# Kernel tuning notes

Hardware: AMD Instinct MI355X
Metric: run time of the kernel (lower is better)

The kernel has to match this reference:

```python
import jax, jax.numpy as jnp
import numpy as np

EPS = 1e-5
NUM_HEADS = 16
HEAD_DIM = 64


def layernorm(x, g, b):
    mu = jnp.mean(x, axis=-1, keepdims=True)
    var = jnp.mean(jnp.square(x - mu), axis=-1, keepdims=True)
    return (x - mu) * jax.lax.rsqrt(var + EPS) * g + b


def setup_inputs() -> dict:
    key = jax.random.key(0)
    ks = jax.random.split(key, 10)
    B, S, Q, D = 4, 4096, 256, 1024
    x = jax.random.normal(ks[0], (B, S, D), dtype=jnp.float32)
    queries = jax.random.normal(ks[1], (B, Q, D), dtype=jnp.float32)
    attn_mask = jax.random.randint(ks[2], (B, NUM_HEADS, Q, S), 0, 2) == 1
    key_padding_mask = jax.random.randint(ks[3], (B, S), 0, 2) == 1
    scale = 1.0 / np.sqrt(2.0 * D)  # xavier-ish
    Wq = jax.random.normal(ks[4], (D, D), dtype=jnp.float32) * scale
    Wk = jax.random.normal(ks[5], (D, D), dtype=jnp.float32) * scale
    Wv = jax.random.normal(ks[6], (D, D), dtype=jnp.float32) * scale
    Wo = jax.random.normal(ks[7], (D, D), dtype=jnp.float32) * scale
    ln1_g = jnp.ones((D,), jnp.float32); ln1_b = jnp.zeros((D,), jnp.float32)
    ln2_g = jnp.ones((D,), jnp.float32); ln2_b = jnp.zeros((D,), jnp.float32)
    return {"x": x, "queries": queries, "attn_mask": attn_mask,
            "key_padding_mask": key_padding_mask, "Wq": Wq, "Wk": Wk,
            "Wv": Wv, "Wo": Wo, "ln1_g": ln1_g, "ln1_b": ln1_b,
            "ln2_g": ln2_g, "ln2_b": ln2_b}


def reference(x, queries, attn_mask, key_padding_mask, Wq, Wk, Wv, Wo,
              ln1_g, ln1_b, ln2_g, ln2_b):
    B, S, D = x.shape
    Q = queries.shape[1]
    H, hd = NUM_HEADS, HEAD_DIM

    xn = layernorm(x, ln1_g, ln1_b)
    q = (queries @ Wq.T).reshape(B, Q, H, hd)
    k = (xn @ Wk.T).reshape(B, S, H, hd)
    v = (xn @ Wv.T).reshape(B, S, H, hd)

    # scores: (B, H, Q, S)
    scores = jnp.einsum('bqhd,bshd->bhqs', q, k) / np.sqrt(hd)

    mask = attn_mask | key_padding_mask[:, None, None, :]
    neg_inf = jnp.float32(-jnp.inf)
    masked = jnp.where(mask, neg_inf, scores)
    all_masked = jnp.all(mask, axis=-1, keepdims=True)  # rows fully masked
    safe = jnp.where(all_masked, 0.0, masked)
    attn = jax.nn.softmax(safe, axis=-1)
    attn = jnp.where(all_masked, 0.0, attn)

    out = jnp.einsum('bhqs,bshd->bqhd', attn, v).reshape(B, Q, D)
    out = layernorm(out, ln2_g, ln2_b)
    return out @ Wo.T, attn.mean(axis=1)
```

## Files before the change

kernel.cpp:

```cpp
#include <hip/hip_runtime.h>
#include <math.h>

#define DEV __device__ __forceinline__

typedef float  f4v  __attribute__((ext_vector_type(4)));
typedef __bf16 b8v  __attribute__((ext_vector_type(8)));
typedef short  s8v  __attribute__((ext_vector_type(8)));

DEV short f2b(float f){ __bf16 h = (__bf16)f; return __builtin_bit_cast(short, h); }
DEV float b2f(short s){ __bf16 h = __builtin_bit_cast(__bf16, s); return (float)h; }

DEV void gload16(const void* g, void* l){
  __builtin_amdgcn_global_load_lds((const __attribute__((address_space(1))) void*)g,
                                   (__attribute__((address_space(3))) void*)l, 16, 0, 0);
}

DEV b8v ldsf(const short* p){ return __builtin_bit_cast(b8v, *(const s8v*)p); }

DEV f4v mfma16(b8v a, b8v b, f4v c){ return __builtin_amdgcn_mfma_f32_16x16x32_bf16(a, b, c, 0, 0, 0); }

DEV void lds_barrier(){
  asm volatile("s_waitcnt lgkmcnt(0)" ::: "memory");
  __builtin_amdgcn_s_barrier();
}

__global__ void cvt5_kernel(const float* __restrict__ s0, const float* __restrict__ s1,
                            const float* __restrict__ s2, const float* __restrict__ s3,
                            const float* __restrict__ s4,
                            short* __restrict__ d0, short* __restrict__ d1,
                            short* __restrict__ d2, short* __restrict__ d3,
                            short* __restrict__ d4){
  int i = blockIdx.x*256 + threadIdx.x;
  int buf = i >> 18, j = i & 262143;
  const float* s = (buf==0)?s0:(buf==1)?s1:(buf==2)?s2:(buf==3)?s3:s4;
  short*       d = (buf==0)?d0:(buf==1)?d1:(buf==2)?d2:(buf==3)?d3:d4;
  float4 v = ((const float4*)s)[j];
  ((short4*)d)[j] = make_short4(f2b(v.x), f2b(v.y), f2b(v.z), f2b(v.w));
}

__global__ __launch_bounds__(256) void ln_kernel(const float* __restrict__ x, const float* __restrict__ gg,
                                                 const float* __restrict__ bb, short* __restrict__ out){
  int row = blockIdx.x, tid = threadIdx.x;
  const float4 v = ((const float4*)(x + (size_t)row*1024))[tid];
  float s = v.x + v.y + v.z + v.w;
  #pragma unroll
  for (int off=1; off<64; off<<=1) s += __shfl_xor(s, off);
  __shared__ float red[4];
  if ((tid&63)==0) red[tid>>6] = s;
  __syncthreads();
  float mu = (red[0]+red[1]+red[2]+red[3]) * (1.0f/1024.0f);
  float d0=v.x-mu, d1=v.y-mu, d2=v.z-mu, d3=v.w-mu;
  float q = d0*d0 + d1*d1 + d2*d2 + d3*d3;
  #pragma unroll
  for (int off=1; off<64; off<<=1) q += __shfl_xor(q, off);
  __syncthreads();
  if ((tid&63)==0) red[tid>>6] = q;
  __syncthreads();
  float rs = rsqrtf((red[0]+red[1]+red[2]+red[3]) * (1.0f/1024.0f) + 1e-5f);
  float4 g4 = ((const float4*)gg)[tid];
  float4 b4 = ((const float4*)bb)[tid];
  short4 o = make_short4(f2b(d0*rs*g4.x + b4.x), f2b(d1*rs*g4.y + b4.y),
                         f2b(d2*rs*g4.z + b4.z), f2b(d3*rs*g4.w + b4.w));
  ((short4*)(out + (size_t)row*1024))[tid] = o;
}

__global__ __launch_bounds__(256) void ln_reduce_kernel(const short* __restrict__ opart, const float* __restrict__ gg,
                                                        const float* __restrict__ bb, short* __restrict__ out){
  int row = blockIdx.x, tid = threadIdx.x;
  float a0=0.f, a1=0.f, a2=0.f, a3=0.f;
  #pragma unroll
  for (int sc=0; sc<16; ++sc){
    short4 t = ((const short4*)(opart + ((size_t)sc*1024 + row)*1024))[tid];
    a0 += b2f(t.x); a1 += b2f(t.y); a2 += b2f(t.z); a3 += b2f(t.w);
  }
  float s = a0 + a1 + a2 + a3;
  #pragma unroll
  for (int off=1; off<64; off<<=1) s += __shfl_xor(s, off);
  __shared__ float red[4];
  if ((tid&63)==0) red[tid>>6] = s;
  __syncthreads();
  float mu = (red[0]+red[1]+red[2]+red[3]) * (1.0f/1024.0f);
  float d0=a0-mu, d1=a1-mu, d2=a2-mu, d3=a3-mu;
  float q = d0*d0 + d1*d1 + d2*d2 + d3*d3;
  #pragma unroll
  for (int off=1; off<64; off<<=1) q += __shfl_xor(q, off);
  __syncthreads();
  if ((tid&63)==0) red[tid>>6] = q;
  __syncthreads();
  float rs = rsqrtf((red[0]+red[1]+red[2]+red[3]) * (1.0f/1024.0f) + 1e-5f);
  float4 g4 = ((const float4*)gg)[tid];
  float4 b4 = ((const float4*)bb)[tid];
  short4 o = make_short4(f2b(d0*rs*g4.x + b4.x), f2b(d1*rs*g4.y + b4.y),
                         f2b(d2*rs*g4.z + b4.z), f2b(d3*rs*g4.w + b4.w));
  ((short4*)(out + (size_t)row*1024))[tid] = o;
}

template<int OUTF32>
__global__ __launch_bounds__(256) void gemm_small(const short* __restrict__ A, const short* __restrict__ B,
                                                  void* __restrict__ C, int M, int N, int K){
  __shared__ short sA[2][64*64];
  __shared__ short sB[2][64*64];
  int tid=threadIdx.x, lane=tid&63, wv=tid>>6, g=lane>>4, r=lane&15;
  int wr=wv>>1, wc=wv&1;
  int m0=blockIdx.x*64, n0=blockIdx.y*64;
  f4v z = {0.f,0.f,0.f,0.f};
  f4v acc[2][2];
  #pragma unroll
  for (int i=0;i<2;++i){
    #pragma unroll
    for (int j=0;j<2;++j) acc[i][j]=z;
  }
  auto stage = [&](int buf, int kt){
    #pragma unroll
    for (int i=0;i<2;++i){
      int idx = i*256 + tid;
      int row = idx>>3, cbs = (idx&7)^(row&7);
      gload16(A + (size_t)(m0+row)*K + kt*64 + cbs*8, &sA[buf][(i*256+wv*64)*8]);
      gload16(B + (size_t)(n0+row)*K + kt*64 + cbs*8, &sB[buf][(i*256+wv*64)*8]);
    }
  };
  int nkt = K >> 6;
  stage(0, 0);
  __syncthreads();
  for (int kt=0; kt<nkt; ++kt){
    int cur = kt & 1;
    if (kt+1 < nkt) stage(cur^1, kt+1);
    b8v af[2][2], bf[2][2];
    #pragma unroll
    for (int mf=0;mf<2;++mf){
      #pragma unroll
      for (int ks=0;ks<2;++ks){
        int ra = wr*32 + mf*16 + r;
        int rb = wc*32 + mf*16 + r;
        af[mf][ks] = ldsf(&sA[cur][ra*64 + (((ks*4+g)^(ra&7))*8)]);
        bf[mf][ks] = ldsf(&sB[cur][rb*64 + (((ks*4+g)^(rb&7))*8)]);
      }
    }
    #pragma unroll
    for (int mf=0;mf<2;++mf){
      #pragma unroll
      for (int nf=0;nf<2;++nf){
        acc[mf][nf] = mfma16(af[mf][0], bf[nf][0], acc[mf][nf]);
        acc[mf][nf] = mfma16(af[mf][1], bf[nf][1], acc[mf][nf]);
      }
    }
    __syncthreads();
  }
  #pragma unroll
  for (int mf=0;mf<2;++mf){
    #pragma unroll
    for (int nf=0;nf<2;++nf){
      #pragma unroll
      for (int j=0;j<4;++j){
        int m = m0 + wr*32 + mf*16 + g*4 + j;
        int n = n0 + wc*32 + nf*16 + r;
        if (OUTF32) ((float*)C)[(size_t)m*N + n] = acc[mf][nf][j];
        else        ((short*)C)[(size_t)m*N + n] = f2b(acc[mf][nf][j]);
      }
    }
  }
}

__global__ __launch_bounds__(512,2) void gemm_dual_bt(const short* __restrict__ A, const short* __restrict__ B0,
                                                      const short* __restrict__ B1, short* __restrict__ C0,
                                                      short* __restrict__ C1, int M, int N, int K){
  __shared__ short sA[2][256*32];
  __shared__ short sB0[2][128*32];
  __shared__ short sB1[2][128*32];
  int tid=threadIdx.x, lane=tid&63, wv=tid>>6, g=lane>>4, r=lane&15;
  int wr=wv>>1, wc=wv&1;
  int m0=blockIdx.x*256, n0=blockIdx.y*128;
  f4v z = {0.f,0.f,0.f,0.f};
  f4v a0[4][4], a1[4][4];
  #pragma unroll
  for (int i=0;i<4;++i){
    #pragma unroll
    for (int j=0;j<4;++j){ a0[i][j]=z; a1[i][j]=z; }
  }
  auto stage = [&](int buf, int kt){
    #pragma unroll
    for (int i=0;i<2;++i){
      int idx = i*512 + tid;
      int row = idx>>2, sl = idx&3;
      gload16(A + (size_t)(m0+row)*K + kt*32 + sl*8, &sA[buf][(i*512+wv*64)*8]);
    }
    {
      int row = tid>>2, sl = tid&3;
      gload16(B0 + (size_t)(n0+row)*K + kt*32 + sl*8, &sB0[buf][(wv*64)*8]);
      gload16(B1 + (size_t)(n0+row)*K + kt*32 + sl*8, &sB1[buf][(wv*64)*8]);
    }
  };
  int nkt = K >> 5;
  stage(0, 0);
  __syncthreads();
  for (int kt=0; kt<nkt; ++kt){
    int cur = kt & 1;
    if (kt+1 < nkt) stage(cur^1, kt+1);
    b8v af[4], b0f[4], b1f[4];
    #pragma unroll
    for (int mf=0;mf<4;++mf) af[mf] = ldsf(&sA[cur][(wr*64+mf*16+r)*32 + g*8]);
    #pragma unroll
    for (int nf=0;nf<4;++nf){
      b0f[nf] = ldsf(&sB0[cur][(wc*64+nf*16+r)*32 + g*8]);
      b1f[nf] = ldsf(&sB1[cur][(wc*64+nf*16+r)*32 + g*8]);
    }
    #pragma unroll
    for (int mf=0;mf<4;++mf){
      #pragma unroll
      for (int nf=0;nf<4;++nf){
        a0[mf][nf] = mfma16(af[mf], b0f[nf], a0[mf][nf]);
        a1[mf][nf] = mfma16(af[mf], b1f[nf], a1[mf][nf]);
      }
    }
    __syncthreads();
  }
  #pragma unroll
  for (int mf=0;mf<4;++mf){
    #pragma unroll
    for (int nf=0;nf<4;++nf){
      #pragma unroll
      for (int j=0;j<4;++j){
        int m = m0 + wr*64 + mf*16 + g*4 + j;
        int n = n0 + wc*64 + nf*16 + r;
        C0[(size_t)m*N + n] = f2b(a0[mf][nf][j]);
        C1[(size_t)m*N + n] = f2b(a1[mf][nf][j]);
      }
    }
  }
}

__global__ __launch_bounds__(256) void vtrans_kernel(const short* __restrict__ v, short* __restrict__ vt){
  int bid = blockIdx.x;
  int sb = bid & 63, bh = bid >> 6;
  int b = bh >> 4, h = bh & 15;
  int s0 = sb*64;
  __shared__ short t[64][80];
  int tid = threadIdx.x;
  #pragma unroll
  for (int i=0;i<2;++i){
    int idx = tid + i*256;
    int row = idx>>3, sl = idx&7;
    *(s8v*)&t[row][sl*8] = *(const s8v*)(v + (size_t)(b*4096 + s0 + row)*1024 + h*64 + sl*8);
  }
  __syncthreads();
  int hd = tid>>2, part = tid&3;
  s8v o0, o1;
  #pragma unroll
  for (int j=0;j<8;++j){ o0[j] = t[part*16+j][hd]; o1[j] = t[part*16+8+j][hd]; }
  size_t base = (size_t)(bh*64+hd)*4096 + s0 + part*16;
  *(s8v*)(vt + base)     = o0;
  *(s8v*)(vt + base + 8) = o1;
}

__global__ __launch_bounds__(256,2) void lsum_kernel(const short* __restrict__ qp, const short* __restrict__ kb,
                                                     const int* __restrict__ am, const int* __restrict__ kpm,
                                                     unsigned* __restrict__ pm, float* __restrict__ lpart){
  int bid = blockIdx.x;
  int sc = bid & 15, bh = bid >> 4;
  int b = bh >> 4, h = bh & 15;
  int s0 = sc*256;
  __shared__ short sQ[256*64];
  __shared__ short sK[256*64];
  __shared__ unsigned sPM[256*8];
  int tid=threadIdx.x, lane=tid&63, wv=tid>>6, g=lane>>4, r=lane&15;

  #pragma unroll
  for (int i=0;i<8;++i){
    int idx = i*256 + wv*64 + lane;
    int row = idx>>3, cbs = (idx&7)^(row&7);
    gload16(qp + (size_t)(b*256 + row)*1024 + h*64 + cbs*8, &sQ[(i*256+wv*64)*8]);
  }
  #pragma unroll
  for (int i=0;i<8;++i){
    int idx = i*256 + wv*64 + lane;
    int row = idx>>3, cbs = (idx&7)^(row&7);
    gload16(kb + (size_t)(b*4096 + s0 + row)*1024 + h*64 + cbs*8, &sK[(i*256+wv*64)*8]);
  }
  int4 kp = *(const int4*)(kpm + (size_t)b*4096 + s0 + lane*4);
  bool k0 = kp.x!=0, k1 = kp.y!=0, k2 = kp.z!=0, k3 = kp.w!=0;
  #pragma unroll 4
  for (int i=0;i<64;++i){
    int row = wv*64 + i;
    const int4 t = *(const int4*)(am + (size_t)(bh*256 + row)*4096 + s0 + lane*4);
    unsigned long long m0 = __ballot(k0 || (t.x!=0));
    unsigned long long m1 = __ballot(k1 || (t.y!=0));
    unsigned long long m2 = __ballot(k2 || (t.z!=0));
    unsigned long long m3 = __ballot(k3 || (t.w!=0));
    if (lane < 8){
      int jj = lane>>1, hh = lane&1;
      unsigned long long bj = (jj==0)?m0:((jj==1)?m1:((jj==2)?m2:m3));
      unsigned w = (unsigned)(bj >> (hh*32));
      sPM[row*8 + lane] = w;
      pm[(size_t)bid*2048 + row*8 + lane] = w;
    }
  }
  __syncthreads();

  b8v a[4][2];
  #pragma unroll
  for (int mf=0;mf<4;++mf){
    #pragma unroll
    for (int ks=0;ks<2;++ks){
      int q = wv*64 + mf*16 + r;
      a[mf][ks] = ldsf(&sQ[q*64 + (((ks*4+g)^(q&7))*8)]);
    }
  }
  unsigned wmr[4][4][2];
  #pragma unroll
  for (int mf=0;mf<4;++mf){
    #pragma unroll
    for (int jq=0;jq<4;++jq){
      int q = wv*64 + mf*16 + g*4 + jq;
      wmr[mf][jq][0] = sPM[q*8 + (r&3)*2 + 0];
      wmr[mf][jq][1] = sPM[q*8 + (r&3)*2 + 1];
    }
  }
  float lacc[4][4];
  #pragma unroll
  for (int mf=0;mf<4;++mf){
    #pragma unroll
    for (int j=0;j<4;++j) lacc[mf][j] = 0.f;
  }
  f4v z = {0.f,0.f,0.f,0.f};
  #pragma unroll 4
  for (int nf=0;nf<16;++nf){
    int srow = nf*16 + r;
    b8v b0 = ldsf(&sK[srow*64 + ((g^(srow&7))*8)]);
    b8v b1 = ldsf(&sK[srow*64 + (((4+g)^(srow&7))*8)]);
    f4v acc[4];
    #pragma unroll
    for (int mf=0;mf<4;++mf){
      acc[mf] = mfma16(a[mf][0], b0, z);
      acc[mf] = mfma16(a[mf][1], b1, acc[mf]);
    }
    int bitp = 4*(nf&7) + (r>>2);
    #pragma unroll
    for (int mf=0;mf<4;++mf){
      #pragma unroll
      for (int j=0;j<4;++j){
        bool mskd = (wmr[mf][j][nf>>3] >> bitp) & 1u;
        lacc[mf][j] += mskd ? 0.f : __expf(acc[mf][j]*0.125f);
      }
    }
  }
  #pragma unroll
  for (int off=1; off<16; off<<=1){
    #pragma unroll
    for (int mf=0;mf<4;++mf){
      #pragma unroll
      for (int j=0;j<4;++j) lacc[mf][j] += __shfl_xor(lacc[mf][j], off);
    }
  }
  if (r == 0){
    #pragma unroll
    for (int mf=0;mf<4;++mf){
      #pragma unroll
      for (int j=0;j<4;++j){
        int q = wv*64 + mf*16 + g*4 + j;
        lpart[(size_t)bid*256 + q] = lacc[mf][j];
      }
    }
  }
}

__global__ void lcomb_kernel(const float* __restrict__ lpart, float* __restrict__ linv){
  int row = blockIdx.x*256 + threadIdx.x;
  int q = row & 255, bh = row >> 8;
  float l = 0.f;
  #pragma unroll
  for (int sc=0; sc<16; ++sc) l += lpart[(size_t)(bh*16+sc)*256 + q];
  linv[row] = (l > 0.f) ? (1.0f/l) : 0.f;
}

__global__ __launch_bounds__(512,2) void attn_pv_kernel(const short* __restrict__ qp, const short* __restrict__ kb,
                                                        const short* __restrict__ vt, const unsigned* __restrict__ pm,
                                                        const float* __restrict__ linv, short* __restrict__ opart,
                                                        float* __restrict__ out2){
  int bid = blockIdx.x;
  int sc = bid & 15, qt = (bid>>4)&3, b = bid>>6;
  int s0 = sc*256, q0 = qt*64;
  __shared__ short sK[2][256*64];
  __shared__ short sV[2][64*256];
  __shared__ short sQ[2][64*64];
  __shared__ unsigned sPM[2][64*8];
  int tid=threadIdx.x, lane=tid&63, wv=tid>>6, g=lane>>4, r=lane&15;
  int wq = wv>>2, ws = wv&3;
  f4v z = {0.f,0.f,0.f,0.f};
  float macc[4][2][4];
  #pragma unroll
  for (int sb=0;sb<4;++sb){
    #pragma unroll
    for (int qb=0;qb<2;++qb){
      #pragma unroll
      for (int j=0;j<4;++j) macc[sb][qb][j] = 0.f;
    }
  }

  auto stage = [&](int buf, int h){
    int bh = b*16 + h;
    { int row = tid>>3, cbs = (tid&7)^(row&7);
      gload16(qp + (size_t)(b*256 + q0 + row)*1024 + h*64 + cbs*8, &sQ[buf][(wv*64)*8]); }
    #pragma unroll
    for (int i=0;i<4;++i){
      int idx = i*512 + tid;
      int row = idx>>3, cbs = (idx&7)^(row&7);
      gload16(kb + (size_t)(b*4096 + s0 + row)*1024 + h*64 + cbs*8, &sK[buf][(i*512+wv*64)*8]);
    }
    #pragma unroll
    for (int i=0;i<4;++i){
      int idx = i*512 + tid;
      int row = idx>>5, sl = idx&31, sls = sl^(row&7);
      gload16(vt + (size_t)(bh*64 + row)*4096 + s0 + sls*8, &sV[buf][(i*512+wv*64)*8]);
    }
  };
  auto pmload = [&](int h)->unsigned {
    return pm[(size_t)((b*16+h)*16+sc)*2048 + (q0 + (tid>>3))*8 + (tid&7)];
  };

  stage(0, 0);
  sPM[0][tid] = pmload(0);
  __syncthreads();

  for (int h=0; h<16; ++h){
    int cur = h&1;
    unsigned pmnext = 0;
    if (h < 15){
      stage(cur^1, h+1);
      pmnext = pmload(h+1);
    }
    int bh = b*16 + h;

    b8v qf[2][2];
    #pragma unroll
    for (int qb=0;qb<2;++qb){
      #pragma unroll
      for (int ks=0;ks<2;++ks){
        int qrow = wq*32 + qb*16 + r;
        qf[qb][ks] = ldsf(&sQ[cur][qrow*64 + (((ks*4+g)^(qrow&7))*8)]);
      }
    }
    f4v accs[4][2];
    #pragma unroll
    for (int sb=0;sb<4;++sb){
      int srow = ws*64 + sb*16 + r;
      b8v k0 = ldsf(&sK[cur][srow*64 + ((g^(srow&7))*8)]);
      b8v k1 = ldsf(&sK[cur][srow*64 + (((4+g)^(srow&7))*8)]);
      #pragma unroll
      for (int qb=0;qb<2;++qb){
        accs[sb][qb] = mfma16(k0, qf[qb][0], z);
        accs[sb][qb] = mfma16(k1, qf[qb][1], accs[sb][qb]);
      }
    }
    lds_barrier();

    float iv[2];
    iv[0] = linv[(size_t)bh*256 + q0 + wq*32 + r];
    iv[1] = linv[(size_t)bh*256 + q0 + wq*32 + 16 + r];
    unsigned wmq[2][4];
    #pragma unroll
    for (int qb=0;qb<2;++qb){
      #pragma unroll
      for (int j=0;j<4;++j)
        wmq[qb][j] = sPM[cur][(wq*32+qb*16+r)*8 + j*2 + (ws>>1)];
    }
    short* P = &sK[cur][0];
    #pragma unroll
    for (int sb=0;sb<4;++sb){
      int bitp = (ws&1)*16 + sb*4 + g;
      #pragma unroll
      for (int qb=0;qb<2;++qb){
        float pj[4];
        #pragma unroll
        for (int j=0;j<4;++j){
          bool mskd = (wmq[qb][j] >> bitp) & 1u;
          pj[j] = mskd ? 0.f : __expf(accs[sb][qb][j]*0.125f) * iv[qb];
          macc[sb][qb][j] += pj[j];
        }
        int q = wq*32 + qb*16 + r;
        unsigned lo = ((unsigned)(unsigned short)f2b(pj[0])) | (((unsigned)(unsigned short)f2b(pj[1]))<<16);
        unsigned hi = ((unsigned)(unsigned short)f2b(pj[2])) | (((unsigned)(unsigned short)f2b(pj[3]))<<16);
        int sbase = (ws*64 + sb*16 + g*4) ^ ((q&7)<<3);
        uint2 pk; pk.x = lo; pk.y = hi;
        *(uint2*)&P[q*256 + sbase] = pk;
      }
    }
    lds_barrier();

    f4v acco[2]; acco[0]=z; acco[1]=z;
    #pragma unroll
    for (int ks=0;ks<8;++ks){
      int vrow = ws*16 + r;
      b8v bv = ldsf(&sV[cur][vrow*256 + (((ks*4+g)^(vrow&7))*8)]);
      #pragma unroll
      for (int mf=0;mf<2;++mf){
        int prow = wq*32 + mf*16 + r;
        b8v ap = ldsf(&P[prow*256 + ((ks*32+g*8) ^ ((prow&7)<<3))]);
        acco[mf] = mfma16(ap, bv, acco[mf]);
      }
    }
    #pragma unroll
    for (int mf=0;mf<2;++mf){
      #pragma unroll
      for (int j=0;j<4;++j)
        opart[((size_t)sc*1024 + b*256 + q0 + wq*32 + mf*16 + g*4 + j)*1024 + h*64 + ws*16 + r] = f2b(acco[mf][j]);
    }
    if (h < 15) sPM[cur^1][tid] = pmnext;
    __syncthreads();
  }

  #pragma unroll
  for (int sb=0;sb<4;++sb){
    #pragma unroll
    for (int qb=0;qb<2;++qb){
      int q = q0 + wq*32 + qb*16 + r;
      float4 o = make_float4(macc[sb][qb][0]*0.0625f, macc[sb][qb][1]*0.0625f,
                             macc[sb][qb][2]*0.0625f, macc[sb][qb][3]*0.0625f);
      *(float4*)&out2[(size_t)(b*256 + q)*4096 + s0 + ws*64 + sb*16 + g*4] = o;
    }
  }
}

extern "C" void kernel_launch(void* const* d_in, const int* in_sizes, int n_in,
                              void* d_out, int out_size, void* d_ws, size_t ws_size,
                              hipStream_t stream){
  const float* x       = (const float*)d_in[0];
  const float* queries = (const float*)d_in[1];
  const int*   am      = (const int*)d_in[2];
  const int*   kpm     = (const int*)d_in[3];
  const float* Wq      = (const float*)d_in[4];
  const float* Wk      = (const float*)d_in[5];
  const float* Wv      = (const float*)d_in[6];
  const float* Wo      = (const float*)d_in[7];
  const float* ln1g    = (const float*)d_in[8];
  const float* ln1b    = (const float*)d_in[9];
  const float* ln2g    = (const float*)d_in[10];
  const float* ln2b    = (const float*)d_in[11];
  float* out0 = (float*)d_out;
  float* out2 = out0 + (size_t)4*256*1024;
  char* ws = (char*)d_ws;

  size_t off = 0;
  auto alloc = [&](size_t bytes){ void* p = ws + off; off += (bytes + 255) & ~(size_t)255; return p; };
  short*    xn   = (short*)alloc(33554432);
  short*    vt   = xn;
  short*    kb   = (short*)alloc(33554432);
  short*    vb   = (short*)alloc(33554432);
  short*    wqb  = (short*)alloc(2097152);
  short*    wkb  = (short*)alloc(2097152);
  short*    wvb  = (short*)alloc(2097152);
  short*    wob  = (short*)alloc(2097152);
  short*    qbf  = (short*)alloc(2097152);
  short*    qpj  = (short*)alloc(2097152);
  unsigned* pmw  = (unsigned*)alloc(8388608);
  float*    lpart= (float*)alloc(1048576);
  float*    linv = (float*)alloc(65536);
  short*    opart= (short*)alloc(33554432);
  short*    onb  = (short*)alloc(2097152);

  cvt5_kernel<<<5120,256,0,stream>>>(queries, Wq, Wk, Wv, Wo, qbf, wqb, wkb, wvb, wob);
  ln_kernel<<<16384,256,0,stream>>>(x, ln1g, ln1b, xn);
  gemm_dual_bt<<<dim3(64,8),512,0,stream>>>(xn, wkb, wvb, kb, vb, 16384, 1024, 1024);
  gemm_small<0><<<dim3(16,16),256,0,stream>>>(qbf, wqb, qpj, 1024, 1024, 1024);
  vtrans_kernel<<<4096,256,0,stream>>>(vb, vt);
  lsum_kernel<<<1024,256,0,stream>>>(qpj, kb, am, kpm, pmw, lpart);
  lcomb_kernel<<<64,256,0,stream>>>(lpart, linv);
  attn_pv_kernel<<<256,512,0,stream>>>(qpj, kb, vt, pmw, linv, opart, out2);
  ln_reduce_kernel<<<1024,256,0,stream>>>(opart, ln2g, ln2b, onb);
  gemm_small<1><<<dim3(16,16),256,0,stream>>>(onb, wob, out0, 1024, 1024, 1024);
}
```

Before: 340.6 us.

## Fuse prep kernels, write V transposed from GEMM epilogue, swizzle LDS, add setprio

Merges the bf16 conversion kernel and the first layernorm into a single launch. The K/V GEMM now writes V directly in the transposed per-head layout, which removes the separate transpose kernel and one 32MB intermediate round trip. The GEMM's LDS tiles get an XOR swizzle to reduce bank conflicts on fragment reads. The attention kernel raises wave priority around its MFMA loops. The transposed V stores are 8-byte strided writes, which may coalesce worse than the old row-major stores.

Result: faster. 328.5 us (-3.5%).

```diff
diff --git a/kernel.cpp b/kernel.cpp
--- a/kernel.cpp
+++ b/kernel.cpp
@@ -24,23 +24,25 @@
   __builtin_amdgcn_s_barrier();
 }
 
-__global__ void cvt5_kernel(const float* __restrict__ s0, const float* __restrict__ s1,
-                            const float* __restrict__ s2, const float* __restrict__ s3,
-                            const float* __restrict__ s4,
-                            short* __restrict__ d0, short* __restrict__ d1,
-                            short* __restrict__ d2, short* __restrict__ d3,
-                            short* __restrict__ d4){
-  int i = blockIdx.x*256 + threadIdx.x;
-  int buf = i >> 18, j = i & 262143;
-  const float* s = (buf==0)?s0:(buf==1)?s1:(buf==2)?s2:(buf==3)?s3:s4;
-  short*       d = (buf==0)?d0:(buf==1)?d1:(buf==2)?d2:(buf==3)?d3:d4;
-  float4 v = ((const float4*)s)[j];
-  ((short4*)d)[j] = make_short4(f2b(v.x), f2b(v.y), f2b(v.z), f2b(v.w));
-}
-
-__global__ __launch_bounds__(256) void ln_kernel(const float* __restrict__ x, const float* __restrict__ gg,
-                                                 const float* __restrict__ bb, short* __restrict__ out){
-  int row = blockIdx.x, tid = threadIdx.x;
+__global__ __launch_bounds__(256) void prep_kernel(const float* __restrict__ x, const float* __restrict__ ln1g,
+                                                   const float* __restrict__ ln1b, short* __restrict__ xn,
+                                                   const float* __restrict__ s0, const float* __restrict__ s1,
+                                                   const float* __restrict__ s2, const float* __restrict__ s3,
+                                                   const float* __restrict__ s4,
+                                                   short* __restrict__ d0, short* __restrict__ d1,
+                                                   short* __restrict__ d2, short* __restrict__ d3,
+                                                   short* __restrict__ d4){
+  int bid = blockIdx.x, tid = threadIdx.x;
+  if (bid < 5120){
+    int i = bid*256 + tid;
+    int buf = i >> 18, j = i & 262143;
+    const float* s = (buf==0)?s0:(buf==1)?s1:(buf==2)?s2:(buf==3)?s3:s4;
+    short*       d = (buf==0)?d0:(buf==1)?d1:(buf==2)?d2:(buf==3)?d3:d4;
+    float4 v = ((const float4*)s)[j];
+    ((short4*)d)[j] = make_short4(f2b(v.x), f2b(v.y), f2b(v.z), f2b(v.w));
+    return;
+  }
+  int row = bid - 5120;
   const float4 v = ((const float4*)(x + (size_t)row*1024))[tid];
   float s = v.x + v.y + v.z + v.w;
   #pragma unroll
@@ -49,19 +51,19 @@
   if ((tid&63)==0) red[tid>>6] = s;
   __syncthreads();
   float mu = (red[0]+red[1]+red[2]+red[3]) * (1.0f/1024.0f);
-  float d0=v.x-mu, d1=v.y-mu, d2=v.z-mu, d3=v.w-mu;
-  float q = d0*d0 + d1*d1 + d2*d2 + d3*d3;
+  float e0=v.x-mu, e1=v.y-mu, e2=v.z-mu, e3=v.w-mu;
+  float q = e0*e0 + e1*e1 + e2*e2 + e3*e3;
   #pragma unroll
   for (int off=1; off<64; off<<=1) q += __shfl_xor(q, off);
   __syncthreads();
   if ((tid&63)==0) red[tid>>6] = q;
   __syncthreads();
   float rs = rsqrtf((red[0]+red[1]+red[2]+red[3]) * (1.0f/1024.0f) + 1e-5f);
-  float4 g4 = ((const float4*)gg)[tid];
-  float4 b4 = ((const float4*)bb)[tid];
-  short4 o = make_short4(f2b(d0*rs*g4.x + b4.x), f2b(d1*rs*g4.y + b4.y),
-                         f2b(d2*rs*g4.z + b4.z), f2b(d3*rs*g4.w + b4.w));
-  ((short4*)(out + (size_t)row*1024))[tid] = o;
+  float4 g4 = ((const float4*)ln1g)[tid];
+  float4 b4 = ((const float4*)ln1b)[tid];
+  short4 o = make_short4(f2b(e0*rs*g4.x + b4.x), f2b(e1*rs*g4.y + b4.y),
+                         f2b(e2*rs*g4.z + b4.z), f2b(e3*rs*g4.w + b4.w));
+  ((short4*)(xn + (size_t)row*1024))[tid] = o;
 }
 
 __global__ __launch_bounds__(256) void ln_reduce_kernel(const short* __restrict__ opart, const float* __restrict__ gg,
@@ -163,7 +165,7 @@
 
 __global__ __launch_bounds__(512,2) void gemm_dual_bt(const short* __restrict__ A, const short* __restrict__ B0,
                                                       const short* __restrict__ B1, short* __restrict__ C0,
-                                                      short* __restrict__ C1, int M, int N, int K){
+                                                      short* __restrict__ vt, int M, int N, int K){
   __shared__ short sA[2][256*32];
   __shared__ short sB0[2][128*32];
   __shared__ short sB1[2][128*32];
@@ -181,11 +183,11 @@
     #pragma unroll
     for (int i=0;i<2;++i){
       int idx = i*512 + tid;
-      int row = idx>>2, sl = idx&3;
+      int row = idx>>2, sl = (idx&3)^(row&3);
       gload16(A + (size_t)(m0+row)*K + kt*32 + sl*8, &sA[buf][(i*512+wv*64)*8]);
     }
     {
-      int row = tid>>2, sl = tid&3;
+      int row = tid>>2, sl = (tid&3)^(row&3);
       gload16(B0 + (size_t)(n0+row)*K + kt*32 + sl*8, &sB0[buf][(wv*64)*8]);
       gload16(B1 + (size_t)(n0+row)*K + kt*32 + sl*8, &sB1[buf][(wv*64)*8]);
     }
@@ -198,11 +200,15 @@
     if (kt+1 < nkt) stage(cur^1, kt+1);
     b8v af[4], b0f[4], b1f[4];
     #pragma unroll
-    for (int mf=0;mf<4;++mf) af[mf] = ldsf(&sA[cur][(wr*64+mf*16+r)*32 + g*8]);
+    for (int mf=0;mf<4;++mf){
+      int ra = wr*64+mf*16+r;
+      af[mf] = ldsf(&sA[cur][ra*32 + ((g^(ra&3))*8)]);
+    }
     #pragma unroll
     for (int nf=0;nf<4;++nf){
-      b0f[nf] = ldsf(&sB0[cur][(wc*64+nf*16+r)*32 + g*8]);
-      b1f[nf] = ldsf(&sB1[cur][(wc*64+nf*16+r)*32 + g*8]);
+      int rb = wc*64+nf*16+r;
+      b0f[nf] = ldsf(&sB0[cur][rb*32 + ((g^(rb&3))*8)]);
+      b1f[nf] = ldsf(&sB1[cur][rb*32 + ((g^(rb&3))*8)]);
     }
     #pragma unroll
     for (int mf=0;mf<4;++mf){
@@ -214,42 +220,22 @@
     }
     __syncthreads();
   }
+  int b = m0 >> 12;
   #pragma unroll
   for (int mf=0;mf<4;++mf){
     #pragma unroll
     for (int nf=0;nf<4;++nf){
-      #pragma unroll
-      for (int j=0;j<4;++j){
-        int m = m0 + wr*64 + mf*16 + g*4 + j;
-        int n = n0 + wc*64 + nf*16 + r;
-        C0[(size_t)m*N + n] = f2b(a0[mf][nf][j]);
-        C1[(size_t)m*N + n] = f2b(a1[mf][nf][j]);
-      }
-    }
-  }
-}
-
-__global__ __launch_bounds__(256) void vtrans_kernel(const short* __restrict__ v, short* __restrict__ vt){
-  int bid = blockIdx.x;
-  int sb = bid & 63, bh = bid >> 6;
-  int b = bh >> 4, h = bh & 15;
-  int s0 = sb*64;
-  __shared__ short t[64][80];
-  int tid = threadIdx.x;
-  #pragma unroll
-  for (int i=0;i<2;++i){
-    int idx = tid + i*256;
-    int row = idx>>3, sl = idx&7;
-    *(s8v*)&t[row][sl*8] = *(const s8v*)(v + (size_t)(b*4096 + s0 + row)*1024 + h*64 + sl*8);
-  }
-  __syncthreads();
-  int hd = tid>>2, part = tid&3;
-  s8v o0, o1;
-  #pragma unroll
-  for (int j=0;j<8;++j){ o0[j] = t[part*16+j][hd]; o1[j] = t[part*16+8+j][hd]; }
-  size_t base = (size_t)(bh*64+hd)*4096 + s0 + part*16;
-  *(s8v*)(vt + base)     = o0;
-  *(s8v*)(vt + base + 8) = o1;
+      int m = m0 + wr*64 + mf*16 + g*4;
+      int n = n0 + wc*64 + nf*16 + r;
+      #pragma unroll
+      for (int j=0;j<4;++j)
+        C0[(size_t)(m+j)*N + n] = f2b(a0[mf][nf][j]);
+      int h = n >> 6, hd = n & 63;
+      short4 vv = make_short4(f2b(a1[mf][nf][0]), f2b(a1[mf][nf][1]),
+                              f2b(a1[mf][nf][2]), f2b(a1[mf][nf][3]));
+      *(short4*)&vt[(size_t)((b*16 + h)*64 + hd)*4096 + (m & 4095)] = vv;
+    }
+  }
 }
 
 __global__ __launch_bounds__(256,2) void lsum_kernel(const short* __restrict__ qp, const short* __restrict__ kb,
@@ -440,6 +426,7 @@
       }
     }
     f4v accs[4][2];
+    __builtin_amdgcn_s_setprio(1);
     #pragma unroll
     for (int sb=0;sb<4;++sb){
       int srow = ws*64 + sb*16 + r;
@@ -451,6 +438,7 @@
         accs[sb][qb] = mfma16(k1, qf[qb][1], accs[sb][qb]);
       }
     }
+    __builtin_amdgcn_s_setprio(0);
     lds_barrier();
 
     float iv[2];
@@ -487,6 +475,7 @@
     lds_barrier();
 
     f4v acco[2]; acco[0]=z; acco[1]=z;
+    __builtin_amdgcn_s_setprio(1);
     #pragma unroll
     for (int ks=0;ks<8;++ks){
       int vrow = ws*16 + r;
@@ -498,6 +487,7 @@
         acco[mf] = mfma16(ap, bv, acco[mf]);
       }
     }
+    __builtin_amdgcn_s_setprio(0);
     #pragma unroll
     for (int mf=0;mf<2;++mf){
       #pragma unroll
@@ -542,9 +532,8 @@
   size_t off = 0;
   auto alloc = [&](size_t bytes){ void* p = ws + off; off += (bytes + 255) & ~(size_t)255; return p; };
   short*    xn   = (short*)alloc(33554432);
-  short*    vt   = xn;
   short*    kb   = (short*)alloc(33554432);
-  short*    vb   = (short*)alloc(33554432);
+  short*    vt   = (short*)alloc(33554432);
   short*    wqb  = (short*)alloc(2097152);
   short*    wkb  = (short*)alloc(2097152);
   short*    wvb  = (short*)alloc(2097152);
@@ -557,11 +546,10 @@
   short*    opart= (short*)alloc(33554432);
   short*    onb  = (short*)alloc(2097152);
 
-  cvt5_kernel<<<5120,256,0,stream>>>(queries, Wq, Wk, Wv, Wo, qbf, wqb, wkb, wvb, wob);
-  ln_kernel<<<16384,256,0,stream>>>(x, ln1g, ln1b, xn);
-  gemm_dual_bt<<<dim3(64,8),512,0,stream>>>(xn, wkb, wvb, kb, vb, 16384, 1024, 1024);
+  prep_kernel<<<21504,256,0,stream>>>(x, ln1g, ln1b, xn,
+                                      queries, Wq, Wk, Wv, Wo, qbf, wqb, wkb, wvb, wob);
+  gemm_dual_bt<<<dim3(64,8),512,0,stream>>>(xn, wkb, wvb, kb, vt, 16384, 1024, 1024);
   gemm_small<0><<<dim3(16,16),256,0,stream>>>(qbf, wqb, qpj, 1024, 1024, 1024);
-  vtrans_kernel<<<4096,256,0,stream>>>(vb, vt);
   lsum_kernel<<<1024,256,0,stream>>>(qpj, kb, am, kpm, pmw, lpart);
   lcomb_kernel<<<64,256,0,stream>>>(lpart, linv);
   attn_pv_kernel<<<256,512,0,stream>>>(qpj, kb, vt, pmw, linv, opart, out2);
```
